# Optimization experiments

Measured on AMD Instinct MI355X. Metric: run time of the kernel, lower is better.

The kernel has to match this reference:

```python
import jax, jax.numpy as jnp
import numpy as np

N_HEAD = 16
ROPE_CACHE = 2500  # Rotary module caches tables of length 2500
NEG_INF = -1e30


def _rope_tables(head_dim):
    inv_freq = 1.0 / (10000.0 ** (jnp.arange(0, head_dim, 2, dtype=jnp.float32) / head_dim))
    t = jnp.arange(ROPE_CACHE, dtype=jnp.float32)
    freqs = t[:, None] * inv_freq[None, :]            # (2500, head_dim//2)
    emb = jnp.concatenate([freqs, freqs], axis=-1)    # (2500, head_dim)
    return jnp.cos(emb), jnp.sin(emb)


def _rotate_half(x):
    h = x.shape[-1] // 2
    return jnp.concatenate([-x[..., h:], x[..., :h]], axis=-1)


def setup_inputs() -> dict:
    key = jax.random.key(0)
    ks = jax.random.split(key, 8)
    B, S, D = 2, 2048, 1024
    H = N_HEAD
    hd = D // H
    return {
        "qx": jax.random.normal(ks[0], (B, S, D), jnp.float32),
        "kvx": jax.random.normal(ks[1], (B, S, D), jnp.float32),
        "k_cache": jnp.zeros((B, H, S, hd), jnp.float32),
        "v_cache": jnp.zeros((B, H, S, hd), jnp.float32),
        "Wq": jax.random.normal(ks[2], (D, D), jnp.float32) * 0.02,
        "bq": jnp.zeros((D,), jnp.float32),
        "Wk": jax.random.normal(ks[3], (D, D), jnp.float32) * 0.02,
        "Wv": jax.random.normal(ks[4], (D, D), jnp.float32) * 0.02,
        "bv": jnp.zeros((D,), jnp.float32),
        "Wo": jax.random.normal(ks[5], (D, D), jnp.float32) * 0.02,
        "bo": jnp.zeros((D,), jnp.float32),
        "q_positions": jnp.arange(S, dtype=jnp.int32),
        "kv_positions": jnp.arange(S, dtype=jnp.int32),
    }


def reference(qx, kvx, k_cache, v_cache, Wq, bq, Wk, Wv, bv, Wo, bo, q_positions, kv_positions):
    B, Sq, D = qx.shape
    H = N_HEAD
    hd = D // H
    Skv = kvx.shape[1]
    cos, sin = _rope_tables(hd)
    # sqrt_qk_scale = sqrt(1) = 1, folded out.

    def rope(x, pos):  # x: (B, S, H, hd)
        c = cos[pos][None, :, None, :]
        s = sin[pos][None, :, None, :]
        return x * c + _rotate_half(x) * s

    # projections (torch Linear: y = x @ W.T + b; key has no bias)
    q = (qx @ Wq.T + bq).reshape(B, Sq, H, hd)
    q = rope(q, q_positions).transpose(0, 2, 1, 3)            # (B,H,Sq,hd)
    k = (kvx @ Wk.T).reshape(B, Skv, H, hd)
    k = rope(k, kv_positions).transpose(0, 2, 1, 3)           # (B,H,Skv,hd)
    v = (kvx @ Wv.T + bv).reshape(B, Skv, H, hd).transpose(0, 2, 1, 3)

    # KV-cache scatter update: k_cache[:, :, kv_positions] = k
    k_cache = k_cache.at[:, :, kv_positions].set(k)
    v_cache = v_cache.at[:, :, kv_positions].set(v)
    Sc = k_cache.shape[2]

    # SDPA (causal), scaled by 1/sqrt(head_dim) as in F.scaled_dot_product_attention
    scores = jnp.einsum('bhqd,bhkd->bhqk', q, k_cache) / jnp.sqrt(jnp.float32(hd))
    causal = jnp.arange(Sq)[:, None] >= jnp.arange(Sc)[None, :]
    scores = jnp.where(causal[None, None], scores, NEG_INF)
    attn = jax.nn.softmax(scores, axis=-1)
    wv = jnp.einsum('bhqk,bhkd->bhqd', attn, v_cache)

    out = wv.transpose(0, 2, 1, 3).reshape(B, Sq, D) @ Wo.T + bo
    return out
```

## Files before the change

kernel.cpp:

```cpp
#include <hip/hip_runtime.h>
#include <cstdint>
#include <cstddef>

#define NH   16
#define SEQ  2048
#define DM   1024
#define HD   64
#define KDIM 1024
#define MROWS 4096

using short8  = __attribute__((ext_vector_type(8))) short;
using short4v = __attribute__((ext_vector_type(4))) short;
using floatx4 = __attribute__((ext_vector_type(4))) float;

__device__ __forceinline__ short f2bf(float f) {
  unsigned int u = __float_as_uint(f);
  u += 0x7fffu + ((u >> 16) & 1u);
  return (short)(u >> 16);
}

__device__ __forceinline__ void async_ld16(const void* g, void* l) {
  __builtin_amdgcn_global_load_lds(
      (const __attribute__((address_space(1))) void*)g,
      (__attribute__((address_space(3))) void*)l, 16, 0, 0);
}

__device__ __forceinline__ float rsum16(float v) {
#pragma unroll
  for (int off = 1; off < 16; off <<= 1) v += __shfl_xor(v, off, 64);
  return v;
}

struct Cvt6 { const float* src[6]; short* dst[6]; int n[6]; };

__global__ void convert6(Cvt6 a) {
  const int which = blockIdx.y;
  const float4* s = (const float4*)a.src[which];
  short4v* d = (short4v*)a.dst[which];
  const int n4 = a.n[which] >> 2;
  const int stride = gridDim.x * blockDim.x;
  for (int i = blockIdx.x * blockDim.x + threadIdx.x; i < n4; i += stride) {
    float4 v = s[i];
    short4v o;
    o.x = f2bf(v.x); o.y = f2bf(v.y); o.z = f2bf(v.z); o.w = f2bf(v.w);
    d[i] = o;
  }
}

__device__ __forceinline__ void gemm_core(const short* __restrict__ A,
                                          const short* __restrict__ B,
                                          int row0, int col0,
                                          short* As, short* Bs,
                                          floatx4 (&acc)[4][4], int tid) {
  const int lane = tid & 63;
  const int w = tid >> 6;
  const int quad = lane >> 4;
  const int ln = lane & 15;
  const int wr = w >> 1, wc = w & 1;

  int rr[2], cc[2];
#pragma unroll
  for (int g = 0; g < 2; ++g) {
    int beta = (w + 4 * g) * 1024 + lane * 16;
    rr[g] = beta >> 6;
    cc[g] = (beta & 63) >> 1;
  }
#pragma unroll
  for (int i = 0; i < 4; ++i)
#pragma unroll
    for (int j = 0; j < 4; ++j) acc[i][j] = (floatx4){0.f, 0.f, 0.f, 0.f};

  for (int k0 = 0; k0 < KDIM; k0 += 32) {
    __syncthreads();
#pragma unroll
    for (int g = 0; g < 2; ++g) {
      async_ld16(A + (size_t)(row0 + rr[g]) * KDIM + k0 + cc[g], As + (w + 4 * g) * 512);
      async_ld16(B + (size_t)(col0 + rr[g]) * KDIM + k0 + cc[g], Bs + (w + 4 * g) * 512);
    }
    __syncthreads();

    short8 af[4], bfr[4];
#pragma unroll
    for (int i = 0; i < 4; ++i)
      af[i] = *(const short8*)(As + (wr * 64 + i * 16 + ln) * 32 + quad * 8);
#pragma unroll
    for (int j = 0; j < 4; ++j)
      bfr[j] = *(const short8*)(Bs + (wc * 64 + j * 16 + ln) * 32 + quad * 8);
#pragma unroll
    for (int i = 0; i < 4; ++i)
#pragma unroll
      for (int j = 0; j < 4; ++j)
        acc[i][j] = __builtin_amdgcn_mfma_f32_16x16x32_bf16(af[i], bfr[j], acc[i][j], 0, 0, 0);
  }
}

__global__ __launch_bounds__(256) void proj_gemm(
    const short* __restrict__ qxb, const short* __restrict__ kvxb,
    const short* __restrict__ Wqb, const short* __restrict__ Wkb,
    const short* __restrict__ Wvb,
    const float* __restrict__ bq, const float* __restrict__ bv,
    short* __restrict__ Qo, short* __restrict__ Ko, short* __restrict__ Vt,
    const int* __restrict__ qpos, const int* __restrict__ kvpos) {
  __shared__ __align__(16) short As[128 * 32];
  __shared__ __align__(16) short Bs[128 * 32];

  const int tid = threadIdx.x;
  const int lane = tid & 63;
  const int w = tid >> 6;
  const int quad = lane >> 4;
  const int ln = lane & 15;
  const int wr = w >> 1, wc = w & 1;
  const int z = blockIdx.z;

  int row0, col0;
  const short *A, *B;
  if (z == 2) {
    A = Wvb; B = kvxb;
    row0 = blockIdx.x * 128;
    col0 = blockIdx.y * 128;
  } else {
    A = z ? kvxb : qxb;
    B = z ? Wkb : Wqb;
    row0 = blockIdx.y * 128;
    col0 = blockIdx.x * 128;
  }

  floatx4 acc[4][4];
  gemm_core(A, B, row0, col0, As, Bs, acc, tid);

  if (z == 2) {
#pragma unroll
    for (int i = 0; i < 4; ++i)
#pragma unroll
      for (int r = 0; r < 4; ++r) {
        int nr = row0 + wr * 64 + i * 16 + quad * 4 + r;
        int h = nr >> 6, d = nr & 63;
        float bb = bv[nr];
        size_t base = ((size_t)(h)*HD + d) * SEQ;
#pragma unroll
        for (int j = 0; j < 4; ++j) {
          int sc = col0 + wc * 64 + j * 16 + ln;
          int b = sc >> 11, s = sc & (SEQ - 1);
          Vt[((size_t)b * NH * HD) * SEQ + base + s] = f2bf(acc[i][j][r] + bb);
        }
      }
  } else {
    const int colbase = col0 + wc * 64;
    const float scale = (z == 0) ? 0.125f : 1.0f;
    const float* bias = (z == 0) ? bq : nullptr;
    const int* pos = (z == 0) ? qpos : kvpos;
    short* Out = (z == 0) ? Qo : Ko;
#pragma unroll
    for (int j = 0; j < 2; ++j) {
      int col1 = colbase + j * 16 + ln;
      float b1 = bias ? bias[col1] : 0.f;
      float b2 = bias ? bias[col1 + 32] : 0.f;
      int h = col1 >> 6;
      int d1 = col1 & 63;
      float fr = __powf(10000.f, -(float)d1 * (1.f / 32.f));
#pragma unroll
      for (int i = 0; i < 4; ++i)
#pragma unroll
        for (int r = 0; r < 4; ++r) {
          int row = row0 + wr * 64 + i * 16 + quad * 4 + r;
          int b = row >> 11, s = row & (SEQ - 1);
          float ang = (float)pos[s] * fr;
          float sn, cs;
          __sincosf(ang, &sn, &cs);
          float x1 = acc[i][j][r] + b1;
          float x2 = acc[i][j + 2][r] + b2;
          float o1 = (x1 * cs - x2 * sn) * scale;
          float o2 = (x2 * cs + x1 * sn) * scale;
          size_t basq = ((((size_t)b * NH + h) * SEQ) + s) * HD;
          Out[basq + d1] = f2bf(o1);
          Out[basq + d1 + 32] = f2bf(o2);
        }
    }
  }
}

__global__ __launch_bounds__(256) void out_gemm(
    const short* __restrict__ Ab, const short* __restrict__ Bb,
    const float* __restrict__ bias, float* __restrict__ out) {
  __shared__ __align__(16) short As[128 * 32];
  __shared__ __align__(16) short Bs[128 * 32];
  const int tid = threadIdx.x;
  const int lane = tid & 63;
  const int w = tid >> 6;
  const int quad = lane >> 4;
  const int ln = lane & 15;
  const int wr = w >> 1, wc = w & 1;
  const int row0 = blockIdx.y * 128;
  const int col0 = blockIdx.x * 128;

  floatx4 acc[4][4];
  gemm_core(Ab, Bb, row0, col0, As, Bs, acc, tid);

#pragma unroll
  for (int j = 0; j < 4; ++j) {
    int col = col0 + wc * 64 + j * 16 + ln;
    float bb = bias[col];
#pragma unroll
    for (int i = 0; i < 4; ++i)
#pragma unroll
      for (int r = 0; r < 4; ++r) {
        int row = row0 + wr * 64 + i * 16 + quad * 4 + r;
        out[(size_t)row * DM + col] = acc[i][j][r] + bb;
      }
  }
}

__global__ __launch_bounds__(128) void attn_kernel(
    const short* __restrict__ Q, const short* __restrict__ Kc,
    const short* __restrict__ Vtg, short* __restrict__ Ov) {
  const int tid = threadIdx.x;
  const int lane = tid & 63;
  const int w = tid >> 6;
  const int quad = lane >> 4;
  const int ln = lane & 15;
  const int bh = blockIdx.y;
  const int bx = blockIdx.x;

  const short* Qb = Q + (size_t)bh * SEQ * HD;
  const short* Kb = Kc + (size_t)bh * SEQ * HD;
  const short* Vb = Vtg + (size_t)bh * HD * SEQ;

  __shared__ __align__(16) short Ks[2 * 64 * 32];
  __shared__ __align__(16) short Vs[2 * 64 * 32];
  __shared__ __align__(16) short Ps[2][32 * 72];

  const int b = bh >> 4, h = bh & 15;

#pragma unroll
  for (int phase = 0; phase < 2; ++phase) {
    const int qt = phase ? bx : (31 - bx);
    const int q0 = qt * 64;
    const int wlo = q0 + w * 32;

    short8 qa[2][2];
#pragma unroll
    for (int i = 0; i < 2; ++i)
#pragma unroll
      for (int kk = 0; kk < 2; ++kk)
        qa[i][kk] = *(const short8*)(Qb + (size_t)(wlo + i * 16 + ln) * HD +
                                     quad * 8 + kk * 32);

    floatx4 oacc[2][4];
    float lp[2][4];
#pragma unroll
    for (int i = 0; i < 2; ++i) {
#pragma unroll
      for (int j = 0; j < 4; ++j) oacc[i][j] = (floatx4){0.f, 0.f, 0.f, 0.f};
#pragma unroll
      for (int r = 0; r < 4; ++r) lp[i][r] = 0.f;
    }

    for (int t = 0; t <= q0; t += 64) {
      __syncthreads();
#pragma unroll
      for (int g = 0; g < 4; ++g) {
        int slot = (w * 4 + g) * 64 + lane;
        int kk = slot >> 8, rowi = (slot >> 2) & 63, grp = slot & 3;
        async_ld16(Kb + (size_t)(t + rowi) * HD + kk * 32 + grp * 8,
                   (char*)Ks + slot * 16);
        async_ld16(Vb + (size_t)rowi * SEQ + t + kk * 32 + grp * 8,
                   (char*)Vs + slot * 16);
      }
      __syncthreads();

      floatx4 sacc[2][4];
#pragma unroll
      for (int i = 0; i < 2; ++i)
#pragma unroll
        for (int j = 0; j < 4; ++j) sacc[i][j] = (floatx4){0.f, 0.f, 0.f, 0.f};
#pragma unroll
      for (int kk = 0; kk < 2; ++kk)
#pragma unroll
        for (int j = 0; j < 4; ++j) {
          short8 kb = *(const short8*)(Ks + kk * 2048 + (j * 16 + ln) * 32 + quad * 8);
          sacc[0][j] = __builtin_amdgcn_mfma_f32_16x16x32_bf16(qa[0][kk], kb, sacc[0][j], 0, 0, 0);
          sacc[1][j] = __builtin_amdgcn_mfma_f32_16x16x32_bf16(qa[1][kk], kb, sacc[1][j], 0, 0, 0);
        }

      const bool need_mask = (t + 63 > wlo);
#pragma unroll
      for (int i = 0; i < 2; ++i)
#pragma unroll
        for (int j = 0; j < 4; ++j)
#pragma unroll
          for (int r = 0; r < 4; ++r) {
            float p = __expf(sacc[i][j][r]);
            if (need_mask) {
              int col = t + j * 16 + ln;
              int row = wlo + i * 16 + quad * 4 + r;
              if (col > row) p = 0.f;
            }
            lp[i][r] += p;
            Ps[w][(i * 16 + quad * 4 + r) * 72 + j * 16 + ln] = f2bf(p);
          }

#pragma unroll
      for (int kk = 0; kk < 2; ++kk) {
        short8 pa0 = *(const short8*)(&Ps[w][(ln) * 72 + quad * 8 + kk * 32]);
        short8 pa1 = *(const short8*)(&Ps[w][(16 + ln) * 72 + quad * 8 + kk * 32]);
#pragma unroll
        for (int j = 0; j < 4; ++j) {
          short8 vb = *(const short8*)(Vs + kk * 2048 + (j * 16 + ln) * 32 + quad * 8);
          oacc[0][j] = __builtin_amdgcn_mfma_f32_16x16x32_bf16(pa0, vb, oacc[0][j], 0, 0, 0);
          oacc[1][j] = __builtin_amdgcn_mfma_f32_16x16x32_bf16(pa1, vb, oacc[1][j], 0, 0, 0);
        }
      }
    }

#pragma unroll
    for (int i = 0; i < 2; ++i)
#pragma unroll
      for (int r = 0; r < 4; ++r) {
        float l = rsum16(lp[i][r]);
        float inv = 1.0f / l;
        int s = wlo + i * 16 + quad * 4 + r;
        size_t base = ((size_t)b * SEQ + s) * DM + h * HD;
#pragma unroll
        for (int j = 0; j < 4; ++j)
          Ov[base + j * 16 + ln] = f2bf(oacc[i][j][r] * inv);
      }
  }
}

extern "C" void kernel_launch(void* const* d_in, const int* in_sizes, int n_in,
                              void* d_out, int out_size, void* d_ws, size_t ws_size,
                              hipStream_t stream) {
  const float* qx  = (const float*)d_in[0];
  const float* kvx = (const float*)d_in[1];
  const float* Wq = (const float*)d_in[4];
  const float* bq = (const float*)d_in[5];
  const float* Wk = (const float*)d_in[6];
  const float* Wv = (const float*)d_in[7];
  const float* bv = (const float*)d_in[8];
  const float* Wo = (const float*)d_in[9];
  const float* bo = (const float*)d_in[10];
  const int* qpos  = (const int*)d_in[11];
  const int* kvpos = (const int*)d_in[12];

  char* ws = (char*)d_ws;
  short* qxb  = (short*)(ws + 0);
  short* kvxb = (short*)(ws + 8388608);
  short* Wqb  = (short*)(ws + 16777216);
  short* Wkb  = (short*)(ws + 18874368);
  short* Wvb  = (short*)(ws + 20971520);
  short* Wob  = (short*)(ws + 23068672);
  short* Qbf  = (short*)(ws + 25165824);
  short* Kbf  = (short*)(ws + 33554432);
  short* Vtb  = (short*)(ws + 41943040);
  short* WVbf = (short*)(ws + 50331648);

  Cvt6 c;
  c.src[0] = qx;  c.dst[0] = qxb;  c.n[0] = MROWS * KDIM;
  c.src[1] = kvx; c.dst[1] = kvxb; c.n[1] = MROWS * KDIM;
  c.src[2] = Wq;  c.dst[2] = Wqb;  c.n[2] = DM * KDIM;
  c.src[3] = Wk;  c.dst[3] = Wkb;  c.n[3] = DM * KDIM;
  c.src[4] = Wv;  c.dst[4] = Wvb;  c.n[4] = DM * KDIM;
  c.src[5] = Wo;  c.dst[5] = Wob;  c.n[5] = DM * KDIM;
  convert6<<<dim3(1024, 6), 256, 0, stream>>>(c);

  proj_gemm<<<dim3(DM / 128, MROWS / 128, 3), 256, 0, stream>>>(
      qxb, kvxb, Wqb, Wkb, Wvb, bq, bv, Qbf, Kbf, Vtb, qpos, kvpos);

  attn_kernel<<<dim3(16, 2 * NH), 128, 0, stream>>>(Qbf, Kbf, Vtb, WVbf);

  out_gemm<<<dim3(DM / 128, MROWS / 128), 256, 0, stream>>>(
      WVbf, Wob, bo, (float*)d_out);
}
```

Measured before the change: 280.6 us.

## Split attention KV loop across blocks and add a partial-sum reduce kernel

Attention no longer pairs two query tiles per block. Each block now handles one query tile and one of two interleaved KV-chunk halves, and writes unnormalized bf16 partial outputs and row sums to workspace. A new reduce kernel adds the partials and normalizes. The QK and PV MFMAs are also transposed so probabilities are stored to LDS as packed short4 and row sums need fewer shuffles. The goal is more blocks in flight and lower LDS store cost, at the price of an extra launch, workspace traffic, per-block load imbalance across tiles, and bf16 rounding of the partials.

```diff
diff --git a/kernel.cpp b/kernel.cpp
--- a/kernel.cpp
+++ b/kernel.cpp
@@ -8,6 +8,7 @@
 #define HD   64
 #define KDIM 1024
 #define MROWS 4096
+#define CH   2
 
 using short8  = __attribute__((ext_vector_type(8))) short;
 using short4v = __attribute__((ext_vector_type(4))) short;
@@ -18,17 +19,14 @@
   u += 0x7fffu + ((u >> 16) & 1u);
   return (short)(u >> 16);
 }
+__device__ __forceinline__ float bf2f(short s) {
+  return __uint_as_float(((unsigned int)(unsigned short)s) << 16);
+}
 
 __device__ __forceinline__ void async_ld16(const void* g, void* l) {
   __builtin_amdgcn_global_load_lds(
       (const __attribute__((address_space(1))) void*)g,
       (__attribute__((address_space(3))) void*)l, 16, 0, 0);
-}
-
-__device__ __forceinline__ float rsum16(float v) {
-#pragma unroll
-  for (int off = 1; off < 16; off <<= 1) v += __shfl_xor(v, off, 64);
-  return v;
 }
 
 struct Cvt6 { const float* src[6]; short* dst[6]; int n[6]; };
@@ -210,9 +208,10 @@
   }
 }
 
-__global__ __launch_bounds__(128) void attn_kernel(
+__global__ __launch_bounds__(128) void attn_partial(
     const short* __restrict__ Q, const short* __restrict__ Kc,
-    const short* __restrict__ Vtg, short* __restrict__ Ov) {
+    const short* __restrict__ Vtg, short* __restrict__ Po,
+    float* __restrict__ Lo) {
   const int tid = threadIdx.x;
   const int lane = tid & 63;
   const int w = tid >> 6;
@@ -220,6 +219,12 @@
   const int ln = lane & 15;
   const int bh = blockIdx.y;
   const int bx = blockIdx.x;
+  const int qt = 31 - (bx >> 1);
+  const int ch = bx & (CH - 1);
+  if (ch > qt) return;
+
+  const int q0 = qt * 64;
+  const int wlo = q0 + w * 32;
 
   const short* Qb = Q + (size_t)bh * SEQ * HD;
   const short* Kb = Kc + (size_t)bh * SEQ * HD;
@@ -227,104 +232,137 @@
 
   __shared__ __align__(16) short Ks[2 * 64 * 32];
   __shared__ __align__(16) short Vs[2 * 64 * 32];
-  __shared__ __align__(16) short Ps[2][32 * 72];
-
-  const int b = bh >> 4, h = bh & 15;
-
-#pragma unroll
-  for (int phase = 0; phase < 2; ++phase) {
-    const int qt = phase ? bx : (31 - bx);
-    const int q0 = qt * 64;
-    const int wlo = q0 + w * 32;
-
-    short8 qa[2][2];
-#pragma unroll
-    for (int i = 0; i < 2; ++i)
-#pragma unroll
-      for (int kk = 0; kk < 2; ++kk)
-        qa[i][kk] = *(const short8*)(Qb + (size_t)(wlo + i * 16 + ln) * HD +
-                                     quad * 8 + kk * 32);
-
-    floatx4 oacc[2][4];
-    float lp[2][4];
-#pragma unroll
-    for (int i = 0; i < 2; ++i) {
-#pragma unroll
-      for (int j = 0; j < 4; ++j) oacc[i][j] = (floatx4){0.f, 0.f, 0.f, 0.f};
-#pragma unroll
-      for (int r = 0; r < 4; ++r) lp[i][r] = 0.f;
+  __shared__ __align__(16) short Pt[2][32 * 72];
+
+  short8 qa[2][2];
+#pragma unroll
+  for (int i = 0; i < 2; ++i)
+#pragma unroll
+    for (int kk = 0; kk < 2; ++kk)
+      qa[i][kk] = *(const short8*)(Qb + (size_t)(wlo + i * 16 + ln) * HD +
+                                   quad * 8 + kk * 32);
+
+  floatx4 oacc[4][2];
+  float lp[2];
+#pragma unroll
+  for (int jd = 0; jd < 4; ++jd)
+#pragma unroll
+    for (int i = 0; i < 2; ++i) oacc[jd][i] = (floatx4){0.f, 0.f, 0.f, 0.f};
+  lp[0] = lp[1] = 0.f;
+
+  for (int t = ch * 64; t <= q0; t += CH * 64) {
+    __syncthreads();
+#pragma unroll
+    for (int g = 0; g < 4; ++g) {
+      int slot = (w * 4 + g) * 64 + lane;
+      int kk = slot >> 8, rowi = (slot >> 2) & 63, grp = slot & 3;
+      async_ld16(Kb + (size_t)(t + rowi) * HD + kk * 32 + grp * 8,
+                 (char*)Ks + slot * 16);
+      async_ld16(Vb + (size_t)rowi * SEQ + t + kk * 32 + grp * 8,
+                 (char*)Vs + slot * 16);
     }
-
-    for (int t = 0; t <= q0; t += 64) {
-      __syncthreads();
-#pragma unroll
-      for (int g = 0; g < 4; ++g) {
-        int slot = (w * 4 + g) * 64 + lane;
-        int kk = slot >> 8, rowi = (slot >> 2) & 63, grp = slot & 3;
-        async_ld16(Kb + (size_t)(t + rowi) * HD + kk * 32 + grp * 8,
-                   (char*)Ks + slot * 16);
-        async_ld16(Vb + (size_t)rowi * SEQ + t + kk * 32 + grp * 8,
-                   (char*)Vs + slot * 16);
+    __syncthreads();
+
+    floatx4 sacc[4][2];
+#pragma unroll
+    for (int c = 0; c < 4; ++c)
+#pragma unroll
+      for (int i = 0; i < 2; ++i) sacc[c][i] = (floatx4){0.f, 0.f, 0.f, 0.f};
+#pragma unroll
+    for (int kk = 0; kk < 2; ++kk)
+#pragma unroll
+      for (int c = 0; c < 4; ++c) {
+        short8 kb = *(const short8*)(Ks + kk * 2048 + (c * 16 + ln) * 32 + quad * 8);
+        sacc[c][0] = __builtin_amdgcn_mfma_f32_16x16x32_bf16(kb, qa[0][kk], sacc[c][0], 0, 0, 0);
+        sacc[c][1] = __builtin_amdgcn_mfma_f32_16x16x32_bf16(kb, qa[1][kk], sacc[c][1], 0, 0, 0);
       }
-      __syncthreads();
-
-      floatx4 sacc[2][4];
-#pragma unroll
-      for (int i = 0; i < 2; ++i)
-#pragma unroll
-        for (int j = 0; j < 4; ++j) sacc[i][j] = (floatx4){0.f, 0.f, 0.f, 0.f};
-#pragma unroll
-      for (int kk = 0; kk < 2; ++kk)
-#pragma unroll
-        for (int j = 0; j < 4; ++j) {
-          short8 kb = *(const short8*)(Ks + kk * 2048 + (j * 16 + ln) * 32 + quad * 8);
-          sacc[0][j] = __builtin_amdgcn_mfma_f32_16x16x32_bf16(qa[0][kk], kb, sacc[0][j], 0, 0, 0);
-          sacc[1][j] = __builtin_amdgcn_mfma_f32_16x16x32_bf16(qa[1][kk], kb, sacc[1][j], 0, 0, 0);
+
+    const bool dmask = (t == q0);
+#pragma unroll
+    for (int c = 0; c < 4; ++c)
+#pragma unroll
+      for (int i = 0; i < 2; ++i) {
+        short4v pk;
+#pragma unroll
+        for (int r = 0; r < 4; ++r) {
+          float p = __expf(sacc[c][i][r]);
+          if (dmask) {
+            int sp = t + c * 16 + quad * 4 + r;
+            int qq = wlo + i * 16 + ln;
+            if (sp > qq) p = 0.f;
+          }
+          lp[i] += p;
+          pk[r] = f2bf(p);
         }
-
-      const bool need_mask = (t + 63 > wlo);
-#pragma unroll
-      for (int i = 0; i < 2; ++i)
-#pragma unroll
-        for (int j = 0; j < 4; ++j)
-#pragma unroll
-          for (int r = 0; r < 4; ++r) {
-            float p = __expf(sacc[i][j][r]);
-            if (need_mask) {
-              int col = t + j * 16 + ln;
-              int row = wlo + i * 16 + quad * 4 + r;
-              if (col > row) p = 0.f;
-            }
-            lp[i][r] += p;
-            Ps[w][(i * 16 + quad * 4 + r) * 72 + j * 16 + ln] = f2bf(p);
-          }
-
-#pragma unroll
-      for (int kk = 0; kk < 2; ++kk) {
-        short8 pa0 = *(const short8*)(&Ps[w][(ln) * 72 + quad * 8 + kk * 32]);
-        short8 pa1 = *(const short8*)(&Ps[w][(16 + ln) * 72 + quad * 8 + kk * 32]);
-#pragma unroll
-        for (int j = 0; j < 4; ++j) {
-          short8 vb = *(const short8*)(Vs + kk * 2048 + (j * 16 + ln) * 32 + quad * 8);
-          oacc[0][j] = __builtin_amdgcn_mfma_f32_16x16x32_bf16(pa0, vb, oacc[0][j], 0, 0, 0);
-          oacc[1][j] = __builtin_amdgcn_mfma_f32_16x16x32_bf16(pa1, vb, oacc[1][j], 0, 0, 0);
-        }
+        *(short4v*)(&Pt[w][(i * 16 + ln) * 72 + c * 16 + quad * 4]) = pk;
+      }
+
+#pragma unroll
+    for (int kk = 0; kk < 2; ++kk) {
+      short8 pb0 = *(const short8*)(&Pt[w][(ln) * 72 + kk * 32 + quad * 8]);
+      short8 pb1 = *(const short8*)(&Pt[w][(16 + ln) * 72 + kk * 32 + quad * 8]);
+#pragma unroll
+      for (int jd = 0; jd < 4; ++jd) {
+        short8 va = *(const short8*)(Vs + kk * 2048 + (jd * 16 + ln) * 32 + quad * 8);
+        oacc[jd][0] = __builtin_amdgcn_mfma_f32_16x16x32_bf16(va, pb0, oacc[jd][0], 0, 0, 0);
+        oacc[jd][1] = __builtin_amdgcn_mfma_f32_16x16x32_bf16(va, pb1, oacc[jd][1], 0, 0, 0);
       }
     }
-
-#pragma unroll
-    for (int i = 0; i < 2; ++i)
-#pragma unroll
-      for (int r = 0; r < 4; ++r) {
-        float l = rsum16(lp[i][r]);
-        float inv = 1.0f / l;
-        int s = wlo + i * 16 + quad * 4 + r;
-        size_t base = ((size_t)b * SEQ + s) * DM + h * HD;
-#pragma unroll
-        for (int j = 0; j < 4; ++j)
-          Ov[base + j * 16 + ln] = f2bf(oacc[i][j][r] * inv);
-      }
-  }
+  }
+
+  const size_t idx = ((size_t)bh * 32 + qt) * CH + ch;
+  short* Pob = Po + idx * 4096;
+#pragma unroll
+  for (int jd = 0; jd < 4; ++jd)
+#pragma unroll
+    for (int i = 0; i < 2; ++i) {
+      short4v pk;
+#pragma unroll
+      for (int r = 0; r < 4; ++r) pk[r] = f2bf(oacc[jd][i][r]);
+      *(short4v*)(Pob + (w * 32 + i * 16 + ln) * 64 + jd * 16 + quad * 4) = pk;
+    }
+#pragma unroll
+  for (int i = 0; i < 2; ++i) {
+    float l = lp[i];
+    l += __shfl_xor(l, 16, 64);
+    l += __shfl_xor(l, 32, 64);
+    if (quad == 0) Lo[idx * 64 + w * 32 + i * 16 + ln] = l;
+  }
+}
+
+__global__ __launch_bounds__(256) void attn_reduce(
+    const short* __restrict__ Po, const float* __restrict__ Lo,
+    short* __restrict__ Ov) {
+  const int qt = blockIdx.x;
+  const int bh = blockIdx.y;
+  const int b = bh >> 4, h = bh & 15;
+  const int tid = threadIdx.x;
+  const int ql = tid >> 2;
+  const int d0 = (tid & 3) * 16;
+  const int nch = (qt >= 1) ? CH : 1;
+  const size_t i0 = ((size_t)bh * 32 + qt) * CH;
+
+  float l = Lo[i0 * 64 + ql];
+  const short8* p0 = (const short8*)(Po + i0 * 4096 + ql * 64 + d0);
+  short8 a0 = p0[0], a1 = p0[1];
+  float acc[16];
+#pragma unroll
+  for (int e = 0; e < 8; ++e) { acc[e] = bf2f(a0[e]); acc[8 + e] = bf2f(a1[e]); }
+  if (nch == 2) {
+    l += Lo[(i0 + 1) * 64 + ql];
+    const short8* p1 = (const short8*)(Po + (i0 + 1) * 4096 + ql * 64 + d0);
+    short8 c0 = p1[0], c1 = p1[1];
+#pragma unroll
+    for (int e = 0; e < 8; ++e) { acc[e] += bf2f(c0[e]); acc[8 + e] += bf2f(c1[e]); }
+  }
+  float inv = 1.f / l;
+  short8 o0, o1;
+#pragma unroll
+  for (int e = 0; e < 8; ++e) { o0[e] = f2bf(acc[e] * inv); o1[e] = f2bf(acc[8 + e] * inv); }
+  int s = qt * 64 + ql;
+  short* dst = Ov + ((size_t)b * SEQ + s) * DM + h * HD + d0;
+  *(short8*)dst = o0;
+  *((short8*)dst + 1) = o1;
 }
 
 extern "C" void kernel_launch(void* const* d_in, const int* in_sizes, int n_in,
@@ -353,6 +391,8 @@
   short* Kbf  = (short*)(ws + 33554432);
   short* Vtb  = (short*)(ws + 41943040);
   short* WVbf = (short*)(ws + 50331648);
+  short* Po = (short*)(ws + 0);
+  float* Lo = (float*)(ws + 16777216);
 
   Cvt6 c;
   c.src[0] = qx;  c.dst[0] = qxb;  c.n[0] = MROWS * KDIM;
@@ -366,7 +406,9 @@
   proj_gemm<<<dim3(DM / 128, MROWS / 128, 3), 256, 0, stream>>>(
       qxb, kvxb, Wqb, Wkb, Wvb, bq, bv, Qbf, Kbf, Vtb, qpos, kvpos);
 
-  attn_kernel<<<dim3(16, 2 * NH), 128, 0, stream>>>(Qbf, Kbf, Vtb, WVbf);
+  attn_partial<<<dim3(32 * CH, 2 * NH), 128, 0, stream>>>(Qbf, Kbf, Vtb, Po, Lo);
+
+  attn_reduce<<<dim3(SEQ / 64, 2 * NH), 256, 0, stream>>>(Po, Lo, WVbf);
 
   out_gemm<<<dim3(DM / 128, MROWS / 128), 256, 0, stream>>>(
       WVbf, Wob, bo, (float*)d_out);
```

After: 265.6 us. -5.3%, faster.
